# Kernel tuning notes

Hardware: AMD Instinct MI355X
Metric: run time of the kernel (lower is better)

Reference implementation:

```python
import jax, jax.numpy as jnp
import numpy as np

N = 100000
E = 1600000
IN_C, HID_C, OUT_C = 128, 128, 64


def setup_inputs() -> dict:
    key = jax.random.key(0)
    ks = jax.random.split(key, 8)
    x = jax.random.normal(ks[0], (N, IN_C), dtype=jnp.float32)
    edge_index = jax.random.randint(ks[1], (2, E), 0, N, dtype=jnp.int64)

    def glorot(k, fan_in, fan_out):
        s = jnp.sqrt(6.0 / (fan_in + fan_out))
        return jax.random.uniform(k, (fan_in, fan_out), jnp.float32, -s, s)

    W1 = glorot(ks[2], IN_C, HID_C)
    b1 = jnp.zeros((HID_C,), jnp.float32)
    W2 = glorot(ks[3], HID_C, HID_C)
    b2 = jnp.zeros((HID_C,), jnp.float32)
    W3 = glorot(ks[4], HID_C, OUT_C)
    b3 = jnp.zeros((OUT_C,), jnp.float32)
    return {"x": x, "edge_index": edge_index,
            "W1": W1, "b1": b1, "W2": W2, "b2": b2, "W3": W3, "b3": b3}


def _gcn_norm(row, col, n_nodes):
    # symmetric normalization, add_self_loops=False (PyG gcn_norm)
    deg = jax.ops.segment_sum(jnp.ones(row.shape[0], jnp.float32), col, num_segments=n_nodes)
    dinv = jnp.where(deg > 0, jax.lax.rsqrt(jnp.maximum(deg, 1.0)), 0.0)
    dinv = jnp.where(deg > 0, deg ** -0.5, 0.0)
    return dinv[row] * dinv[col]  # [E]


def _gcn_conv(x, row, col, norm, W, b):
    h = x @ W                                # [N, F_out] dense GEMM first (PyG order)
    msg = h[row] * norm[:, None]             # gather + scale, [E, F_out]
    out = jax.ops.segment_sum(msg, col, num_segments=x.shape[0])  # scatter-add
    return out + b


def reference(x, edge_index, W1, b1, W2, b2, W3, b3):
    row, col = edge_index[0], edge_index[1]
    norm = _gcn_norm(row, col, x.shape[0])
    h = jax.nn.relu(_gcn_conv(x, row, col, norm, W1, b1))   # dropout is identity in eval
    h = jax.nn.relu(_gcn_conv(h, row, col, norm, W2, b2))
    out = _gcn_conv(h, row, col, norm, W3, b3)
    return out
```

## Files before the change

### kernel.cpp

```cpp
#include <hip/hip_runtime.h>
#include <hip/hip_bf16.h>
#include <hip/hip_fp16.h>


#define K_DIM 128
#define SCAN_CHUNK 1024

typedef _Float16 f16x8 __attribute__((ext_vector_type(8)));
typedef float f32x4 __attribute__((ext_vector_type(4)));
struct h2s { _Float16 x, y; };

static inline long long cdiv_ll(long long a, long long b) { return (a + b - 1) / b; }

__global__ __launch_bounds__(256) void count_kernel(const int* __restrict__ col, int* __restrict__ cnt,
                                                    int* __restrict__ rank, int E) {
    int e = blockIdx.x * 256 + threadIdx.x;
    if (e < E) rank[e] = atomicAdd(&cnt[col[e]], 1);
}

__global__ __launch_bounds__(256) void dinv_kernel(const int* __restrict__ cnt, float* __restrict__ dinv, int N) {
    int n = blockIdx.x * 256 + threadIdx.x;
    if (n < N) {
        int d = cnt[n];
        dinv[n] = (d > 0) ? (1.0f / sqrtf((float)d)) : 0.0f;
    }
}

__global__ __launch_bounds__(256) void scan1_kernel(const int* __restrict__ cnt, int* __restrict__ off,
                                                    int* __restrict__ bsum, int N) {
    __shared__ int lds[256];
    const int t = threadIdx.x;
    const int base = blockIdx.x * SCAN_CHUNK;
    int v[4], s = 0;
#pragma unroll
    for (int j = 0; j < 4; ++j) {
        int i = base + t * 4 + j;
        v[j] = (i < N) ? cnt[i] : 0;
        s += v[j];
    }
    lds[t] = s;
    __syncthreads();
    for (int d = 1; d < 256; d <<= 1) {
        int x = (t >= d) ? lds[t - d] : 0;
        __syncthreads();
        lds[t] += x;
        __syncthreads();
    }
    int excl = lds[t] - s;
    if (t == 255) bsum[blockIdx.x] = lds[255];
    int run = excl;
#pragma unroll
    for (int j = 0; j < 4; ++j) {
        int i = base + t * 4 + j;
        if (i < N) off[i] = run;
        run += v[j];
    }
}

__global__ __launch_bounds__(256) void scan2_kernel(int* __restrict__ bsum, int G, int* __restrict__ off,
                                                    int N, int E) {
    __shared__ int lds[256];
    const int t = threadIdx.x;
    int s = (t < G) ? bsum[t] : 0;
    lds[t] = s;
    __syncthreads();
    for (int d = 1; d < 256; d <<= 1) {
        int x = (t >= d) ? lds[t - d] : 0;
        __syncthreads();
        lds[t] += x;
        __syncthreads();
    }
    if (t < G) bsum[t] = lds[t] - s;
    if (t == 0) off[N] = E;
}

__global__ __launch_bounds__(256) void scan3_kernel(int* __restrict__ off, const int* __restrict__ bsum, int N) {
    int add = bsum[blockIdx.x];
    const int base = blockIdx.x * SCAN_CHUNK;
#pragma unroll
    for (int j = 0; j < 4; ++j) {
        int i = base + threadIdx.x * 4 + j;
        if (i < N) off[i] += add;
    }
}

__global__ __launch_bounds__(256) void fill_kernel(const int* __restrict__ row, const int* __restrict__ col,
                                                   const int* __restrict__ off, const int* __restrict__ rank,
                                                   int* __restrict__ csr_row, int E) {
    int e = blockIdx.x * 256 + threadIdx.x;
    if (e < E) {
        int idx = off[col[e]] + rank[e];
        __builtin_nontemporal_store(row[e], &csr_row[idx]);
    }
}

template <int COUT>
__global__ __launch_bounds__(256) void pack_w_kernel(const float* __restrict__ W, _Float16* __restrict__ Wp) {
    constexpr int NT = COUT / 16;
    int t = blockIdx.x * 256 + threadIdx.x;
    if (t >= 4 * NT * 64) return;
    int lane = t & 63;
    int nt = (t >> 6) % NT;
    int kt = t / (64 * NT);
    int c = lane & 15, q = lane >> 4;
    f16x8 v;
#pragma unroll
    for (int j = 0; j < 8; ++j) {
        int k = kt * 32 + q * 8 + j;
        v[j] = (_Float16)W[k * COUT + nt * 16 + c];
    }
    *(f16x8*)&Wp[(size_t)t * 8] = v;
}

template <int COUT, bool AF16>
__global__ __launch_bounds__(256) void gemm_mfma(const void* __restrict__ Av, const _Float16* __restrict__ Wp,
                                                 const float* __restrict__ dinv, _Float16* __restrict__ Cmat, int M) {
    constexpr int NT = COUT / 16;
    constexpr int NFRAG = 4 * NT * 64;
    __shared__ _Float16 Wlds[NFRAG * 8];

    const int t = threadIdx.x;
    for (int i = t; i < NFRAG; i += 256)
        *(f16x8*)&Wlds[(size_t)i * 8] = *(const f16x8*)&Wp[(size_t)i * 8];
    __syncthreads();

    const int lane = t & 63;
    const int wave = t >> 6;
    const int c = lane & 15;
    const int q = lane >> 4;
    const int row_base = blockIdx.x * 128 + wave * 32;

    f32x4 acc[2][NT];
#pragma unroll
    for (int rt = 0; rt < 2; ++rt)
#pragma unroll
        for (int nt = 0; nt < NT; ++nt) {
            acc[rt][nt][0] = 0.f; acc[rt][nt][1] = 0.f;
            acc[rt][nt][2] = 0.f; acc[rt][nt][3] = 0.f;
        }

#pragma unroll
    for (int kt = 0; kt < 4; ++kt) {
        f16x8 a[2];
#pragma unroll
        for (int rt = 0; rt < 2; ++rt) {
            int r = row_base + rt * 16 + c;
            r = (r < M) ? r : (M - 1);
            if (AF16) {
                const _Float16* Ap = (const _Float16*)Av;
                int p = kt * 2 + (q >> 1);
                a[rt] = *(const f16x8*)&Ap[((size_t)p * M + r) * 16 + (q & 1) * 8];
            } else {
                const float* ap = (const float*)Av + (size_t)r * K_DIM + kt * 32 + q * 8;
                float4 v0 = *(const float4*)ap;
                float4 v1 = *(const float4*)(ap + 4);
                f16x8 av;
                av[0] = (_Float16)v0.x; av[1] = (_Float16)v0.y;
                av[2] = (_Float16)v0.z; av[3] = (_Float16)v0.w;
                av[4] = (_Float16)v1.x; av[5] = (_Float16)v1.y;
                av[6] = (_Float16)v1.z; av[7] = (_Float16)v1.w;
                a[rt] = av;
            }
        }
#pragma unroll
        for (int nt = 0; nt < NT; ++nt) {
            f16x8 b = *(const f16x8*)&Wlds[(size_t)((kt * NT + nt) * 64 + lane) * 8];
            acc[0][nt] = __builtin_amdgcn_mfma_f32_16x16x32_f16(a[0], b, acc[0][nt], 0, 0, 0);
            acc[1][nt] = __builtin_amdgcn_mfma_f32_16x16x32_f16(a[1], b, acc[1][nt], 0, 0, 0);
        }
    }

#pragma unroll
    for (int rt = 0; rt < 2; ++rt)
#pragma unroll
        for (int reg = 0; reg < 4; ++reg) {
            int row = row_base + rt * 16 + q * 4 + reg;
            if (row < M) {
                float dv = dinv[row];
#pragma unroll
                for (int nt = 0; nt < NT; ++nt)
                    Cmat[((size_t)nt * M + row) * 16 + c] = (_Float16)(acc[rt][nt][reg] * dv);
            }
        }
}

template <int NP, bool RELU, typename OutT>
__global__ __launch_bounds__(256) void gather_lds(const _Float16* __restrict__ g, const int* __restrict__ off,
                                                  const int* __restrict__ csr_row, const float* __restrict__ dinv,
                                                  const float* __restrict__ bias, OutT* __restrict__ outp, int N) {
    constexpr int NTILE = 32;
    constexpr int CH = 512;
    __shared__ _Float16 feat[CH * 16];
    __shared__ int off_s[NTILE + 1];

    const int t = threadIdx.x;
    const int plane = blockIdx.x % NP;
    const int node0 = (blockIdx.x / NP) * NTILE;
    const _Float16* gp = g + (size_t)plane * N * 16;

    if (t <= NTILE) {
        int idx = node0 + t;
        off_s[t] = off[idx < N ? idx : N];
    }
    __syncthreads();

    const int n_loc = t >> 3;
    const int q = t & 7;
    const int node = node0 + n_loc;
    const bool valid = node < N;
    const int sn0 = off_s[n_loc];
    const int sn1 = off_s[n_loc + 1];
    const int s_begin = off_s[0];
    const int s_end = off_s[NTILE];

    float ax = 0.f, ay = 0.f;

    for (int cs = s_begin; cs < s_end; cs += CH) {
        const int ce = (cs + CH < s_end) ? (cs + CH) : s_end;
        const int cnt = ce - cs;
        for (int i = t; i < cnt; i += 256) {
            int r = csr_row[cs + i];
            const _Float16* src = gp + (size_t)r * 16;
            f16x8 lo = *(const f16x8*)src;
            f16x8 hi = *(const f16x8*)(src + 8);
            *(f16x8*)&feat[i * 16] = lo;
            *(f16x8*)&feat[i * 16 + 8] = hi;
        }
        __syncthreads();
        const int lo_s = (sn0 > cs) ? sn0 : cs;
        const int hi_s = (sn1 < ce) ? sn1 : ce;
        for (int s = lo_s; s < hi_s; ++s) {
            h2s v = *(const h2s*)&feat[(s - cs) * 16 + q * 2];
            ax += (float)v.x;
            ay += (float)v.y;
        }
        __syncthreads();
    }

    if (valid) {
        float dv = dinv[node];
        float ox = ax * dv + bias[plane * 16 + q * 2 + 0];
        float oy = ay * dv + bias[plane * 16 + q * 2 + 1];
        if (RELU) { ox = fmaxf(ox, 0.f); oy = fmaxf(oy, 0.f); }
        if constexpr (sizeof(OutT) == 2) {
            h2s o; o.x = (_Float16)ox; o.y = (_Float16)oy;
            *(h2s*)((_Float16*)outp + ((size_t)plane * N + node) * 16 + q * 2) = o;
        } else {
            float2 o = make_float2(ox, oy);
            *(float2*)((float*)outp + (size_t)node * 64 + plane * 16 + q * 2) = o;
        }
    }
}

extern "C" void kernel_launch(void* const* d_in, const int* in_sizes, int n_in,
                              void* d_out, int out_size, void* d_ws, size_t ws_size,
                              hipStream_t stream) {
    const float* x  = (const float*)d_in[0];
    const int*   ei = (const int*)d_in[1];
    const float* W1 = (const float*)d_in[2];
    const float* b1 = (const float*)d_in[3];
    const float* W2 = (const float*)d_in[4];
    const float* b2 = (const float*)d_in[5];
    const float* W3 = (const float*)d_in[6];
    const float* b3 = (const float*)d_in[7];

    const int N = in_sizes[0] / 128;
    const int E = in_sizes[1] / 2;
    const int* row = ei;
    const int* col = ei + E;
    const int G = (int)cdiv_ll(N, SCAN_CHUNK);

    char* wsb = (char*)d_ws;
    int*      cnt     = (int*)wsb;      wsb += (size_t)N * 4;
    float*    dinv    = (float*)wsb;    wsb += (size_t)N * 4;
    int*      off     = (int*)wsb;      wsb += (size_t)(N + 1) * 4;
    int*      bsum    = (int*)wsb;      wsb += 256 * 4;
    int*      rank    = (int*)wsb;      wsb += (size_t)E * 4;
    int*      csr_row = (int*)wsb;      wsb += (size_t)E * 4;
    wsb = (char*)((((uintptr_t)wsb) + 15) & ~(uintptr_t)15);
    _Float16* Wp1     = (_Float16*)wsb; wsb += 16384 * 2;
    _Float16* Wp2     = (_Float16*)wsb; wsb += 16384 * 2;
    _Float16* Wp3     = (_Float16*)wsb; wsb += 8192 * 2;
    _Float16* bufA    = (_Float16*)wsb; wsb += (size_t)N * 128 * 2;
    _Float16* bufB    = (_Float16*)wsb;
    float*    out     = (float*)d_out;

    hipMemsetAsync(cnt, 0, (size_t)N * 4, stream);
    count_kernel<<<cdiv_ll(E, 256), 256, 0, stream>>>(col, cnt, rank, E);
    dinv_kernel<<<cdiv_ll(N, 256), 256, 0, stream>>>(cnt, dinv, N);
    scan1_kernel<<<G, 256, 0, stream>>>(cnt, off, bsum, N);
    scan2_kernel<<<1, 256, 0, stream>>>(bsum, G, off, N, E);
    scan3_kernel<<<G, 256, 0, stream>>>(off, bsum, N);
    fill_kernel<<<cdiv_ll(E, 256), 256, 0, stream>>>(row, col, off, rank, csr_row, E);
    pack_w_kernel<128><<<8, 256, 0, stream>>>(W1, Wp1);
    pack_w_kernel<128><<<8, 256, 0, stream>>>(W2, Wp2);
    pack_w_kernel<64><<<4, 256, 0, stream>>>(W3, Wp3);

    const long long gemmBlocks = cdiv_ll(N, 128);
    const long long nb         = cdiv_ll(N, 32);

    gemm_mfma<128, false><<<gemmBlocks, 256, 0, stream>>>(x, Wp1, dinv, bufA, N);
    gather_lds<8, true, _Float16><<<nb * 8, 256, 0, stream>>>(bufA, off, csr_row, dinv, b1, bufB, N);

    gemm_mfma<128, true><<<gemmBlocks, 256, 0, stream>>>(bufB, Wp2, dinv, bufA, N);
    gather_lds<8, true, _Float16><<<nb * 8, 256, 0, stream>>>(bufA, off, csr_row, dinv, b2, bufB, N);

    gemm_mfma<64, true><<<gemmBlocks, 256, 0, stream>>>(bufB, Wp3, dinv, bufA, N);
    gather_lds<4, false, float><<<nb * 4, 256, 0, stream>>>(bufA, off, csr_row, dinv, b3, out, N);
}
```

Baseline: 491.7 us.

## Switch feature buffers to row-major and gather full rows via global_load_lds

Replaces the planar 16-wide feature layout with row-major [N, COUT] storage in both the GEMM output and input paths. The aggregation kernel now has one block handle all columns for a tile of nodes, and copies each neighbor's full row straight into LDS with 16-byte global_load_lds. Each thread then accumulates 8 channels. The goal is to stop re-reading csr_row and re-walking the edge list once per plane, and to make each neighbor fetch a contiguous row. The catch is larger LDS per block and a dependence on correct LDS addressing for the direct-to-LDS loads. The GEMM A loads also become plain row-major loads.

```diff
diff --git a/kernel.cpp b/kernel.cpp
--- a/kernel.cpp
+++ b/kernel.cpp
@@ -8,7 +8,8 @@
 
 typedef _Float16 f16x8 __attribute__((ext_vector_type(8)));
 typedef float f32x4 __attribute__((ext_vector_type(4)));
-struct h2s { _Float16 x, y; };
+typedef const __attribute__((address_space(1))) void gbl_void;
+typedef __attribute__((address_space(3))) void lds_void;
 
 static inline long long cdiv_ll(long long a, long long b) { return (a + b - 1) / b; }
 
@@ -148,8 +149,7 @@
             r = (r < M) ? r : (M - 1);
             if (AF16) {
                 const _Float16* Ap = (const _Float16*)Av;
-                int p = kt * 2 + (q >> 1);
-                a[rt] = *(const f16x8*)&Ap[((size_t)p * M + r) * 16 + (q & 1) * 8];
+                a[rt] = *(const f16x8*)&Ap[(size_t)r * K_DIM + kt * 32 + q * 8];
             } else {
                 const float* ap = (const float*)Av + (size_t)r * K_DIM + kt * 32 + q * 8;
                 float4 v0 = *(const float4*)ap;
@@ -179,24 +179,25 @@
                 float dv = dinv[row];
 #pragma unroll
                 for (int nt = 0; nt < NT; ++nt)
-                    Cmat[((size_t)nt * M + row) * 16 + c] = (_Float16)(acc[rt][nt][reg] * dv);
+                    Cmat[(size_t)row * COUT + nt * 16 + c] = (_Float16)(acc[rt][nt][reg] * dv);
             }
         }
 }
 
-template <int NP, bool RELU, typename OutT>
-__global__ __launch_bounds__(256) void gather_lds(const _Float16* __restrict__ g, const int* __restrict__ off,
+template <int COUT, bool RELU, typename OutT>
+__global__ __launch_bounds__(256) void gather_row(const _Float16* __restrict__ g, const int* __restrict__ off,
                                                   const int* __restrict__ csr_row, const float* __restrict__ dinv,
                                                   const float* __restrict__ bias, OutT* __restrict__ outp, int N) {
-    constexpr int NTILE = 32;
-    constexpr int CH = 512;
-    __shared__ _Float16 feat[CH * 16];
+    constexpr int TPN = COUT / 8;
+    constexpr int NTILE = 256 / TPN;
+    constexpr int CH = 16384 / COUT;
+    constexpr int EPI = 256 / TPN;
+    constexpr int EPW = 64 / TPN;
+    __shared__ _Float16 feat[CH * COUT];
     __shared__ int off_s[NTILE + 1];
 
     const int t = threadIdx.x;
-    const int plane = blockIdx.x % NP;
-    const int node0 = (blockIdx.x / NP) * NTILE;
-    const _Float16* gp = g + (size_t)plane * N * 16;
+    const int node0 = blockIdx.x * NTILE;
 
     if (t <= NTILE) {
         int idx = node0 + t;
@@ -204,8 +205,9 @@
     }
     __syncthreads();
 
-    const int n_loc = t >> 3;
-    const int q = t & 7;
+    const int j = t % TPN;
+    const int n_loc = t / TPN;
+    const int w = t >> 6;
     const int node = node0 + n_loc;
     const bool valid = node < N;
     const int sn0 = off_s[n_loc];
@@ -213,41 +215,52 @@
     const int s_begin = off_s[0];
     const int s_end = off_s[NTILE];
 
-    float ax = 0.f, ay = 0.f;
+    float acc[8];
+#pragma unroll
+    for (int k = 0; k < 8; ++k) acc[k] = 0.f;
 
     for (int cs = s_begin; cs < s_end; cs += CH) {
         const int ce = (cs + CH < s_end) ? (cs + CH) : s_end;
         const int cnt = ce - cs;
-        for (int i = t; i < cnt; i += 256) {
-            int r = csr_row[cs + i];
-            const _Float16* src = gp + (size_t)r * 16;
-            f16x8 lo = *(const f16x8*)src;
-            f16x8 hi = *(const f16x8*)(src + 8);
-            *(f16x8*)&feat[i * 16] = lo;
-            *(f16x8*)&feat[i * 16 + 8] = hi;
+        const int kmax = (cnt + EPI - 1) / EPI;
+        for (int k = 0; k < kmax; ++k) {
+            int i = k * EPI + n_loc;
+            if (i < cnt) {
+                int r = csr_row[cs + i];
+                const _Float16* src = g + (size_t)r * COUT + j * 8;
+                __builtin_amdgcn_global_load_lds((gbl_void*)src,
+                                                 (lds_void*)&feat[(size_t)(k * EPI + w * EPW) * COUT],
+                                                 16, 0, 0);
+            }
         }
         __syncthreads();
         const int lo_s = (sn0 > cs) ? sn0 : cs;
         const int hi_s = (sn1 < ce) ? sn1 : ce;
         for (int s = lo_s; s < hi_s; ++s) {
-            h2s v = *(const h2s*)&feat[(s - cs) * 16 + q * 2];
-            ax += (float)v.x;
-            ay += (float)v.y;
+            f16x8 v = *(const f16x8*)&feat[(size_t)(s - cs) * COUT + j * 8];
+#pragma unroll
+            for (int k = 0; k < 8; ++k) acc[k] += (float)v[k];
         }
         __syncthreads();
     }
 
     if (valid) {
         float dv = dinv[node];
-        float ox = ax * dv + bias[plane * 16 + q * 2 + 0];
-        float oy = ay * dv + bias[plane * 16 + q * 2 + 1];
-        if (RELU) { ox = fmaxf(ox, 0.f); oy = fmaxf(oy, 0.f); }
+        float o[8];
+#pragma unroll
+        for (int k = 0; k < 8; ++k) {
+            o[k] = acc[k] * dv + bias[j * 8 + k];
+            if (RELU) o[k] = fmaxf(o[k], 0.f);
+        }
         if constexpr (sizeof(OutT) == 2) {
-            h2s o; o.x = (_Float16)ox; o.y = (_Float16)oy;
-            *(h2s*)((_Float16*)outp + ((size_t)plane * N + node) * 16 + q * 2) = o;
+            f16x8 h;
+#pragma unroll
+            for (int k = 0; k < 8; ++k) h[k] = (_Float16)o[k];
+            *(f16x8*)((_Float16*)outp + (size_t)node * COUT + j * 8) = h;
         } else {
-            float2 o = make_float2(ox, oy);
-            *(float2*)((float*)outp + (size_t)node * 64 + plane * 16 + q * 2) = o;
+            float* op = (float*)outp + (size_t)node * COUT + j * 8;
+            *(float4*)op = make_float4(o[0], o[1], o[2], o[3]);
+            *(float4*)(op + 4) = make_float4(o[4], o[5], o[6], o[7]);
         }
     }
 }
@@ -297,14 +310,13 @@
     pack_w_kernel<64><<<4, 256, 0, stream>>>(W3, Wp3);
 
     const long long gemmBlocks = cdiv_ll(N, 128);
-    const long long nb         = cdiv_ll(N, 32);
 
     gemm_mfma<128, false><<<gemmBlocks, 256, 0, stream>>>(x, Wp1, dinv, bufA, N);
-    gather_lds<8, true, _Float16><<<nb * 8, 256, 0, stream>>>(bufA, off, csr_row, dinv, b1, bufB, N);
+    gather_row<128, true, _Float16><<<cdiv_ll(N, 16), 256, 0, stream>>>(bufA, off, csr_row, dinv, b1, bufB, N);
 
     gemm_mfma<128, true><<<gemmBlocks, 256, 0, stream>>>(bufB, Wp2, dinv, bufA, N);
-    gather_lds<8, true, _Float16><<<nb * 8, 256, 0, stream>>>(bufA, off, csr_row, dinv, b2, bufB, N);
+    gather_row<128, true, _Float16><<<cdiv_ll(N, 16), 256, 0, stream>>>(bufA, off, csr_row, dinv, b2, bufB, N);
 
     gemm_mfma<64, true><<<gemmBlocks, 256, 0, stream>>>(bufB, Wp3, dinv, bufA, N);
-    gather_lds<4, false, float><<<nb * 4, 256, 0, stream>>>(bufA, off, csr_row, dinv, b3, out, N);
-}
+    gather_row<64, false, float><<<cdiv_ll(N, 32), 256, 0, stream>>>(bufA, off, csr_row, dinv, b3, out, N);
+}
```

New measurement: 517.4 us. +5.2%, slower.
